# Performance work log

Hardware: AMD Instinct MI355X
Metric: run time of the kernel (lower is better)

## Reference

```python
import jax, jax.numpy as jnp
import numpy as np

H, C = 4, 32          # num_heads, hidden_channels
NEG_ATT = 0.2         # GAT attention leaky_relu slope (PyG default)
NEG_ACT = 0.01        # F.leaky_relu default slope applied after each conv


def gat_conv(x_src, x_dst, Wsrc, Wdst, a_src, a_dst, bias, src_idx, dst_idx, n_dst):
    """One bipartite GATConv (add_self_loops=False, concat=True)."""
    hs = (x_src @ Wsrc).reshape(-1, H, C)            # [Ns,H,C]
    hd = (x_dst @ Wdst).reshape(-1, H, C)            # [Nd,H,C]
    a_s = (hs * a_src).sum(-1)                       # [Ns,H]
    a_d = (hd * a_dst).sum(-1)                       # [Nd,H]
    e = jax.nn.leaky_relu(a_s[src_idx] + a_d[dst_idx], NEG_ATT)  # [E,H]
    m = jax.ops.segment_max(e, dst_idx, num_segments=n_dst)      # [Nd,H]
    ex = jnp.exp(e - m[dst_idx])
    denom = jax.ops.segment_sum(ex, dst_idx, num_segments=n_dst)
    alpha = ex / (denom[dst_idx] + 1e-16)            # edge softmax over dst
    msg = hs[src_idx] * alpha[:, :, None]            # [E,H,C]
    out = jax.ops.segment_sum(msg, dst_idx, num_segments=n_dst)  # [Nd,H,C]
    return out.reshape(n_dst, H * C) + bias


def setup_inputs() -> dict:
    key = jax.random.key(0)
    ks = jax.random.split(key, 40)
    it = iter(range(40))
    Nu, Nm, E, D, O = 100000, 20000, 500000, 64, 64
    HC = H * C

    def rn(shape, s=0.1):
        return jax.random.normal(ks[next(it)], shape, jnp.float32) * s

    def ri(n, hi):
        return jax.random.randint(ks[next(it)], (n,), 0, hi)

    return {
        "user_ids": jnp.arange(Nu), "movie_ids": jnp.arange(Nm),
        "um_src": ri(E, Nu), "um_dst": ri(E, Nm),
        "mu_src": ri(E, Nm), "mu_dst": ri(E, Nu),
        "user_emb": rn((Nu, D)), "movie_emb": rn((Nm, D)),
        "l1_um_Wsrc": rn((D, HC)), "l1_um_Wdst": rn((D, HC)),
        "l1_um_asrc": rn((H, C)), "l1_um_adst": rn((H, C)), "l1_um_b": rn((HC,)),
        "l1_mu_Wsrc": rn((D, HC)), "l1_mu_Wdst": rn((D, HC)),
        "l1_mu_asrc": rn((H, C)), "l1_mu_adst": rn((H, C)), "l1_mu_b": rn((HC,)),
        "l2_um_W": rn((HC, HC)), "l2_um_asrc": rn((H, C)), "l2_um_adst": rn((H, C)), "l2_um_b": rn((HC,)),
        "l2_mu_W": rn((HC, HC)), "l2_mu_asrc": rn((H, C)), "l2_mu_adst": rn((H, C)), "l2_mu_b": rn((HC,)),
        "Wo": rn((HC, O)), "bo": rn((O,)),
    }


def reference(user_ids, movie_ids, um_src, um_dst, mu_src, mu_dst,
              user_emb, movie_emb,
              l1_um_Wsrc, l1_um_Wdst, l1_um_asrc, l1_um_adst, l1_um_b,
              l1_mu_Wsrc, l1_mu_Wdst, l1_mu_asrc, l1_mu_adst, l1_mu_b,
              l2_um_W, l2_um_asrc, l2_um_adst, l2_um_b,
              l2_mu_W, l2_mu_asrc, l2_mu_adst, l2_mu_b,
              Wo, bo):
    xu = user_emb[user_ids]
    xm = movie_emb[movie_ids]
    Nu, Nm = xu.shape[0], xm.shape[0]
    # layer 1 (HeteroConv sum: each dst type receives exactly one edge type here)
    hm = gat_conv(xu, xm, l1_um_Wsrc, l1_um_Wdst, l1_um_asrc, l1_um_adst, l1_um_b, um_src, um_dst, Nm)
    hu = gat_conv(xm, xu, l1_mu_Wsrc, l1_mu_Wdst, l1_mu_asrc, l1_mu_adst, l1_mu_b, mu_src, mu_dst, Nu)
    xu = jax.nn.leaky_relu(hu, NEG_ACT)
    xm = jax.nn.leaky_relu(hm, NEG_ACT)
    # layer 2 (non-bipartite in_channels int => shared lin for src and dst)
    hm = gat_conv(xu, xm, l2_um_W, l2_um_W, l2_um_asrc, l2_um_adst, l2_um_b, um_src, um_dst, Nm)
    hu = gat_conv(xm, xu, l2_mu_W, l2_mu_W, l2_mu_asrc, l2_mu_adst, l2_mu_b, mu_src, mu_dst, Nu)
    xu = jax.nn.leaky_relu(hu, NEG_ACT)
    xm = jax.nn.leaky_relu(hm, NEG_ACT)
    out_user = xu @ Wo + bo
    out_movie = xm @ Wo + bo
    return out_user, out_movie, xu, xm
```

## Files before the change

kernel.cpp:

```cpp
#include <hip/hip_runtime.h>
#include <hip/hip_bf16.h>
#include <cstdint>


#define HC 128
#define HH 4
#define WPART 256
#define EPB 2048

typedef __attribute__((ext_vector_type(8))) short bf16x8;
typedef __attribute__((ext_vector_type(4))) float f32x4;

__device__ __forceinline__ short f2bf(float f) {
    return __builtin_bit_cast(short, __float2bfloat16(f));
}
__device__ __forceinline__ float bf2f(ushort u) {
    return __builtin_bit_cast(float, ((unsigned)u) << 16);
}

struct VT { const float* W[8]; const float* a[8]; float* v[8]; };
__global__ void make_v_all_k(VT t) {
    int gid = blockIdx.x * 256 + threadIdx.x;
    int task, base;
    if (gid < 1024) { task = gid >> 8; base = gid & 255; }
    else if (gid < 3072) { int g = gid - 1024; task = 4 + (g >> 9); base = g & 511; }
    else return;
    int k = base >> 2, h = base & 3;
    int coff = (task & 1) * 4;
    const float* wr = t.W[task] + (size_t)k * HC + h * 32;
    const float* ar = t.a[task] + h * 32;
    float s = 0.f;
    #pragma unroll
    for (int c = 0; c < 32; ++c) s = fmaf(wr[c], ar[c], s);
    t.v[task][k * 8 + coff + h] = s;
}

struct PT { const float* W[5]; const float* V[5]; ushort* Wb[5];
            int K[5]; int Nw[5]; int start[6]; };
__global__ void pack_all_k(PT t) {
    int gid = blockIdx.x * 256 + threadIdx.x;
    if (gid >= t.start[5]) return;
    int task = 0;
    while (gid >= t.start[task + 1]) ++task;
    int loc = gid - t.start[task];
    int K = t.K[task], Nw = t.Nw[task];
    int n = loc / K, k = loc % K;
    float v = 0.f;
    if (n < Nw) v = t.W[task][(size_t)k * Nw + n];
    else if (t.V[task] != nullptr && n < Nw + 8) v = t.V[task][k * 8 + (n - Nw)];
    t.Wb[task][loc] = (ushort)f2bf(v);
}

template <int NT, int MODE, bool ABF>
__global__ __launch_bounds__(256) void gemm_dual_k(
    const void* A0, const int* idx0, const ushort* Wb0, ushort* hsb0,
    ushort* atts0, float* attd0, float* C0, const float* bias0, int M0, int nb0,
    const void* A1, const int* idx1, const ushort* Wb1, ushort* hsb1,
    ushort* atts1, float* attd1, float* C1, const float* bias1, int M1,
    int K, int ldc) {
    const void* A; const int* aidx; const ushort* Wb; ushort* hsb;
    ushort* atts; float* attd; float* C; const float* bias; int M, bid;
    if ((int)blockIdx.x < nb0) {
        A = A0; aidx = idx0; Wb = Wb0; hsb = hsb0; atts = atts0; attd = attd0;
        C = C0; bias = bias0; M = M0; bid = blockIdx.x;
    } else {
        A = A1; aidx = idx1; Wb = Wb1; hsb = hsb1; atts = atts1; attd = attd1;
        C = C1; bias = bias1; M = M1; bid = blockIdx.x - nb0;
    }
    int lane = threadIdx.x & 63;
    int wave = threadIdx.x >> 6;
    int m_base = bid * 128 + wave * 32;
    int lm = lane & 15;
    int kg = lane >> 4;

    int r0 = m_base + lm, r1 = r0 + 16;
    int cr0 = r0 < M ? r0 : M - 1;
    int cr1 = r1 < M ? r1 : M - 1;
    int row0 = aidx ? aidx[cr0] : cr0;
    int row1 = aidx ? aidx[cr1] : cr1;
    const ushort* bp = Wb + (size_t)lm * K + kg * 8;

    f32x4 acc[2][NT] = {};
    for (int k0 = 0; k0 < K; k0 += 32) {
        bf16x8 a[2];
        if (ABF) {
            const ushort* a0p = (const ushort*)A + (size_t)row0 * K + kg * 8;
            const ushort* a1p = (const ushort*)A + (size_t)row1 * K + kg * 8;
            a[0] = *reinterpret_cast<const bf16x8*>(a0p + k0);
            a[1] = *reinterpret_cast<const bf16x8*>(a1p + k0);
        } else {
            const float* a0p = (const float*)A + (size_t)row0 * K + kg * 8;
            const float* a1p = (const float*)A + (size_t)row1 * K + kg * 8;
            float af[2][8];
            *reinterpret_cast<float4*>(&af[0][0]) = *reinterpret_cast<const float4*>(a0p + k0);
            *reinterpret_cast<float4*>(&af[0][4]) = *reinterpret_cast<const float4*>(a0p + k0 + 4);
            *reinterpret_cast<float4*>(&af[1][0]) = *reinterpret_cast<const float4*>(a1p + k0);
            *reinterpret_cast<float4*>(&af[1][4]) = *reinterpret_cast<const float4*>(a1p + k0 + 4);
            #pragma unroll
            for (int mi = 0; mi < 2; ++mi)
                #pragma unroll
                for (int j = 0; j < 8; ++j) a[mi][j] = f2bf(af[mi][j]);
        }
        #pragma unroll
        for (int nt = 0; nt < NT; ++nt) {
            bf16x8 b = *reinterpret_cast<const bf16x8*>(bp + (size_t)nt * 16 * K + k0);
            acc[0][nt] = __builtin_amdgcn_mfma_f32_16x16x32_bf16(a[0], b, acc[0][nt], 0, 0, 0);
            acc[1][nt] = __builtin_amdgcn_mfma_f32_16x16x32_bf16(a[1], b, acc[1][nt], 0, 0, 0);
        }
    }
    #pragma unroll
    for (int mi = 0; mi < 2; ++mi) {
        int rowb = m_base + mi * 16 + kg * 4;
        if (MODE == 0) {
            #pragma unroll
            for (int nt = 0; nt < NT - 1; ++nt) {
                int col = nt * 16 + lm;
                #pragma unroll
                for (int r = 0; r < 4; ++r) {
                    int row = rowb + r;
                    if (row < M) hsb[(size_t)row * HC + col] = (ushort)f2bf(acc[mi][nt][r]);
                }
            }
            #pragma unroll
            for (int r = 0; r < 4; ++r) {
                int row = rowb + r;
                if (row < M) {
                    float v = acc[mi][NT - 1][r];
                    if (lm < 4) atts[(size_t)row * 4 + lm] = (ushort)f2bf(v);
                    else if (lm < 8) attd[(size_t)row * 4 + (lm - 4)] = v;
                }
            }
        } else {
            #pragma unroll
            for (int nt = 0; nt < NT; ++nt) {
                int col = nt * 16 + lm;
                float bv = bias[col];
                #pragma unroll
                for (int r = 0; r < 4; ++r) {
                    int row = rowb + r;
                    if (row < M) C[(size_t)row * ldc + col] = acc[mi][nt][r] + bv;
                }
            }
        }
    }
}

__global__ __launch_bounds__(256) void part_count_k(
    const int* __restrict__ d0, int E0,
    const int* __restrict__ d1, int E1, int Nm,
    int* __restrict__ cntmat, int NB1) {
    __shared__ int lh[WPART];
    int t = threadIdx.x;
    lh[t] = 0;
    __syncthreads();
    int base = blockIdx.x * EPB + t;
    #pragma unroll
    for (int j = 0; j < EPB / 256; ++j) {
        int e = base + j * 256;
        int key = -1;
        if (e < E0) key = d0[e];
        else if (e - E0 < E1) key = Nm + d1[e - E0];
        if (key >= 0) atomicAdd(&lh[key >> 9], 1);
    }
    __syncthreads();
    cntmat[(size_t)t * NB1 + blockIdx.x] = lh[t];
}

__global__ __launch_bounds__(256) void part_scatter_k(
    const int* __restrict__ s0, const int* __restrict__ d0, int E0,
    const int* __restrict__ s1, const int* __restrict__ d1, int E1, int Nm,
    const int* __restrict__ scanned, int NB1, int2* __restrict__ buf) {
    __shared__ int lb[WPART];
    __shared__ int lc[WPART];
    int t = threadIdx.x;
    lb[t] = scanned[(size_t)t * NB1 + blockIdx.x];
    lc[t] = 0;
    __syncthreads();
    int base = blockIdx.x * EPB + t;
    #pragma unroll
    for (int j = 0; j < EPB / 256; ++j) {
        int e = base + j * 256;
        int key = -1, src = 0;
        if (e < E0) { key = d0[e]; src = s0[e]; }
        else if (e - E0 < E1) { key = Nm + d1[e - E0]; src = s1[e - E0]; }
        if (key >= 0) {
            int w = key >> 9;
            int r = atomicAdd(&lc[w], 1);
            buf[lb[w] + r] = make_int2(src, key);
        }
    }
}

__global__ __launch_bounds__(512) void csort_k(
    const int2* __restrict__ buf, const int* __restrict__ scanned, int NB1,
    int E, int NK, int* __restrict__ rs, int* __restrict__ csr) {
    __shared__ int c1[512];
    __shared__ int ls[512];
    int b = blockIdx.x;
    int t = threadIdx.x;
    int lo = scanned[(size_t)b * NB1];
    int hi = (b + 1 < WPART) ? scanned[(size_t)(b + 1) * NB1] : E;
    int keylo = b << 9;
    c1[t] = 0;
    __syncthreads();
    for (int i = lo + t; i < hi; i += 512)
        atomicAdd(&c1[buf[i].y - keylo], 1);
    __syncthreads();
    int v = c1[t];
    ls[t] = v;
    __syncthreads();
    for (int off = 1; off < 512; off <<= 1) {
        int x = (t >= off) ? ls[t - off] : 0;
        __syncthreads();
        ls[t] += x;
        __syncthreads();
    }
    ls[t] -= v;
    int gk = keylo + t;
    if (gk <= NK) rs[gk] = lo + ls[t];
    c1[t] = 0;
    __syncthreads();
    for (int i = lo + t; i < hi; i += 512) {
        int2 p = buf[i];
        int k = p.y - keylo;
        int r = atomicAdd(&c1[k], 1);
        csr[lo + ls[k] + r] = p.x;
    }
}

__global__ void scan_block_k(const int* __restrict__ deg, int n,
                             int* __restrict__ out, int* __restrict__ partial) {
    __shared__ int s[256];
    int i = blockIdx.x * 256 + threadIdx.x;
    int v = (i < n) ? deg[i] : 0;
    s[threadIdx.x] = v;
    __syncthreads();
    for (int off = 1; off < 256; off <<= 1) {
        int x = (threadIdx.x >= off) ? s[threadIdx.x - off] : 0;
        __syncthreads();
        s[threadIdx.x] += x;
        __syncthreads();
    }
    if (i < n) out[i] = s[threadIdx.x] - v;
    if (threadIdx.x == 255) partial[blockIdx.x] = s[255];
}

__global__ void scan_partial_k(int* __restrict__ partial, int nb) {
    __shared__ int s[512];
    int t = threadIdx.x;
    int v = (t < nb) ? partial[t] : 0;
    s[t] = v;
    __syncthreads();
    for (int off = 1; off < 512; off <<= 1) {
        int x = (t >= off) ? s[t - off] : 0;
        __syncthreads();
        s[t] += x;
        __syncthreads();
    }
    if (t < nb) partial[t] = s[t] - v;
}

__global__ void add_off_k(int* __restrict__ out, const int* __restrict__ partial, int n) {
    int i = blockIdx.x * 256 + threadIdx.x;
    if (i < n) out[i] += partial[blockIdx.x];
}

template <bool WF32, bool PROJ, bool GEMM2>
__global__ __launch_bounds__(256) void agg16_dual_k(
    const int* __restrict__ rs0, const int* __restrict__ csr0,
    const ushort* __restrict__ hsb0, const ushort* __restrict__ atts0,
    const float* __restrict__ attd0, const float* __restrict__ bias0,
    float* __restrict__ out0, int n0,
    const int* __restrict__ rs1, const int* __restrict__ csr1,
    const ushort* __restrict__ hsb1, const ushort* __restrict__ atts1,
    const float* __restrict__ attd1, const float* __restrict__ bias1,
    float* __restrict__ out1, int n1,
    const ushort* __restrict__ Wbo, const float* __restrict__ bo,
    float* __restrict__ pj0, float* __restrict__ pj1,
    const ushort* __restrict__ W2_0, ushort* __restrict__ hs2_0,
    ushort* __restrict__ atts2_0, float* __restrict__ attd2_0,
    const ushort* __restrict__ W2_1, ushort* __restrict__ hs2_1,
    ushort* __restrict__ atts2_1, float* __restrict__ attd2_1) {
    int blocksM = (n0 + 15) >> 4;
    bool ty1 = (int)blockIdx.x >= blocksM;
    int base = ty1 ? ((int)blockIdx.x - blocksM) * 16 : (int)blockIdx.x * 16;
    int gl = threadIdx.x >> 4;
    int c  = threadIdx.x & 15;
    int h  = c >> 2;
    const int* rs = ty1 ? rs1 : rs0;
    const int* csr = ty1 ? csr1 : csr0;
    const ushort* hsb = ty1 ? hsb1 : hsb0;
    const ushort* atts = ty1 ? atts1 : atts0;
    const float* attd = ty1 ? attd1 : attd0;
    const float* bias = ty1 ? bias1 : bias0;
    int n = ty1 ? n1 : n0;
    int node = base + gl;
    bool active = node < n;
    int nodeC = active ? node : 0;

    float ad = attd[nodeC * 4 + h];
    int s0 = 0, s1 = 0;
    if (active) { s0 = rs[nodeC]; s1 = rs[nodeC + 1]; }
    float acc[8] = {};
    float wsum = 0.f;
    int i = s0;
    for (; i + 4 <= s1; i += 4) {
        int sx[4];
        #pragma unroll
        for (int j = 0; j < 4; ++j) sx[j] = csr[i + j];
        bf16x8 hv[4]; float el[4];
        #pragma unroll
        for (int j = 0; j < 4; ++j) {
            hv[j] = *reinterpret_cast<const bf16x8*>(hsb + (size_t)sx[j] * HC + 8 * c);
            el[j] = bf2f(atts[(size_t)sx[j] * 4 + h]);
        }
        #pragma unroll
        for (int j = 0; j < 4; ++j) {
            float e = el[j] + ad;
            e = e > 0.f ? e : 0.2f * e;
            float w = __expf(e);
            wsum += w;
            #pragma unroll
            for (int k = 0; k < 8; ++k)
                acc[k] = fmaf(w, bf2f((ushort)hv[j][k]), acc[k]);
        }
    }
    for (; i < s1; ++i) {
        int src = csr[i];
        bf16x8 hv = *reinterpret_cast<const bf16x8*>(hsb + (size_t)src * HC + 8 * c);
        float e = bf2f(atts[(size_t)src * 4 + h]) + ad;
        e = e > 0.f ? e : 0.2f * e;
        float w = __expf(e);
        wsum += w;
        #pragma unroll
        for (int k = 0; k < 8; ++k)
            acc[k] = fmaf(w, bf2f((ushort)hv[k]), acc[k]);
    }
    float inv = 1.f / (wsum + 1e-16f);
    float v[8];
    #pragma unroll
    for (int k = 0; k < 8; ++k) {
        v[k] = fmaf(acc[k], inv, bias[8 * c + k]);
        v[k] = v[k] > 0.f ? v[k] : 0.01f * v[k];
    }
    if (WF32 && active) {
        float* out = ty1 ? out1 : out0;
        float4 o0 = make_float4(v[0], v[1], v[2], v[3]);
        float4 o1 = make_float4(v[4], v[5], v[6], v[7]);
        reinterpret_cast<float4*>(out + (size_t)node * HC + 8 * c)[0] = o0;
        reinterpret_cast<float4*>(out + (size_t)node * HC + 8 * c)[1] = o1;
    }
    if constexpr (PROJ || GEMM2) {
        __shared__ ushort As[16][136];
        bf16x8 u;
        #pragma unroll
        for (int k = 0; k < 8; ++k) u[k] = active ? f2bf(v[k]) : (short)0;
        *reinterpret_cast<bf16x8*>(&As[gl][8 * c]) = u;
        __syncthreads();
        int lane = threadIdx.x & 63;
        int wv = threadIdx.x >> 6;
        int lm = lane & 15;
        int kg = lane >> 4;
        if constexpr (PROJ) {
            int col = wv * 16 + lm;
            const ushort* bp = Wbo + (size_t)col * HC + kg * 8;
            f32x4 pacc = {};
            #pragma unroll
            for (int k0 = 0; k0 < HC; k0 += 32) {
                bf16x8 a = *reinterpret_cast<const bf16x8*>(&As[lm][k0 + kg * 8]);
                bf16x8 b = *reinterpret_cast<const bf16x8*>(bp + k0);
                pacc = __builtin_amdgcn_mfma_f32_16x16x32_bf16(a, b, pacc, 0, 0, 0);
            }
            float bv = bo[col];
            float* pj = ty1 ? pj1 : pj0;
            #pragma unroll
            for (int r = 0; r < 4; ++r) {
                int nd = base + kg * 4 + r;
                if (nd < n) pj[(size_t)nd * 64 + col] = pacc[r] + bv;
            }
        }
        if constexpr (GEMM2) {
            const ushort* W2 = ty1 ? W2_1 : W2_0;
            ushort* hs2 = ty1 ? hs2_1 : hs2_0;
            ushort* atts2 = ty1 ? atts2_1 : atts2_0;
            float* attd2 = ty1 ? attd2_1 : attd2_0;
            #pragma unroll
            for (int ti = 0; ti < 3; ++ti) {
                int t = wv + ti * 4;
                if (t > 8) break;
                int col = t * 16 + lm;
                const ushort* bp = W2 + (size_t)col * HC + kg * 8;
                f32x4 gacc = {};
                #pragma unroll
                for (int k0 = 0; k0 < HC; k0 += 32) {
                    bf16x8 a = *reinterpret_cast<const bf16x8*>(&As[lm][k0 + kg * 8]);
                    bf16x8 b = *reinterpret_cast<const bf16x8*>(bp + k0);
                    gacc = __builtin_amdgcn_mfma_f32_16x16x32_bf16(a, b, gacc, 0, 0, 0);
                }
                #pragma unroll
                for (int r = 0; r < 4; ++r) {
                    int nd = base + kg * 4 + r;
                    if (nd < n) {
                        if (t < 8) {
                            hs2[(size_t)nd * HC + col] = (ushort)f2bf(gacc[r]);
                        } else {
                            if (lm < 4) atts2[(size_t)nd * 4 + lm] = (ushort)f2bf(gacc[r]);
                            else if (lm < 8) attd2[(size_t)nd * 4 + (lm - 4)] = gacc[r];
                        }
                    }
                }
            }
        }
    }
}

extern "C" void kernel_launch(void* const* d_in, const int* in_sizes, int n_in,
                              void* d_out, int out_size, void* d_ws, size_t ws_size,
                              hipStream_t stream) {
    const int Nu = in_sizes[0];
    const int Nm = in_sizes[1];
    const int E1 = in_sizes[2];
    const int E2 = in_sizes[4];
    const int D  = in_sizes[6] / Nu;
    const int O  = in_sizes[27];
    const int E  = E1 + E2;
    const int NK = Nm + Nu;

    const int*   user_ids  = (const int*)d_in[0];
    const int*   movie_ids = (const int*)d_in[1];
    const int*   um_src    = (const int*)d_in[2];
    const int*   um_dst    = (const int*)d_in[3];
    const int*   mu_src    = (const int*)d_in[4];
    const int*   mu_dst    = (const int*)d_in[5];
    const float* user_emb  = (const float*)d_in[6];
    const float* movie_emb = (const float*)d_in[7];
    const float* l1_um_Wsrc = (const float*)d_in[8];
    const float* l1_um_Wdst = (const float*)d_in[9];
    const float* l1_um_asrc = (const float*)d_in[10];
    const float* l1_um_adst = (const float*)d_in[11];
    const float* l1_um_b    = (const float*)d_in[12];
    const float* l1_mu_Wsrc = (const float*)d_in[13];
    const float* l1_mu_Wdst = (const float*)d_in[14];
    const float* l1_mu_asrc = (const float*)d_in[15];
    const float* l1_mu_adst = (const float*)d_in[16];
    const float* l1_mu_b    = (const float*)d_in[17];
    const float* l2_um_W    = (const float*)d_in[18];
    const float* l2_um_asrc = (const float*)d_in[19];
    const float* l2_um_adst = (const float*)d_in[20];
    const float* l2_um_b    = (const float*)d_in[21];
    const float* l2_mu_W    = (const float*)d_in[22];
    const float* l2_mu_asrc = (const float*)d_in[23];
    const float* l2_mu_adst = (const float*)d_in[24];
    const float* l2_mu_b    = (const float*)d_in[25];
    const float* Wo         = (const float*)d_in[26];
    const float* bo         = (const float*)d_in[27];

    auto cdiv = [](int a, int b) { return (a + b - 1) / b; };
    const int NB1 = cdiv(E, EPB);
    const int CM  = WPART * NB1;

    char* p = (char*)d_ws;
    auto alloc = [&](size_t bytes) { void* r = p; p += (bytes + 255) & ~(size_t)255; return r; };
    ushort* hs_u  = (ushort*)alloc((size_t)Nu * HC * 2);
    ushort* hs_m  = (ushort*)alloc((size_t)Nm * HC * 2);
    ushort* hs_u2 = (ushort*)alloc((size_t)Nu * HC * 2);
    ushort* hs_m2 = (ushort*)alloc((size_t)Nm * HC * 2);
    ushort* atts_u  = (ushort*)alloc((size_t)Nu * 4 * 2);
    ushort* atts_m  = (ushort*)alloc((size_t)Nm * 4 * 2);
    ushort* atts_u2 = (ushort*)alloc((size_t)Nu * 4 * 2);
    ushort* atts_m2 = (ushort*)alloc((size_t)Nm * 4 * 2);
    float* attd_u  = (float*)alloc((size_t)Nu * 4 * 4);
    float* attd_m  = (float*)alloc((size_t)Nm * 4 * 4);
    float* attd_u2 = (float*)alloc((size_t)Nu * 4 * 4);
    float* attd_m2 = (float*)alloc((size_t)Nm * 4 * 4);
    float* V_u1  = (float*)alloc((size_t)HC * 8 * 4);
    float* V_m1  = (float*)alloc((size_t)HC * 8 * 4);
    float* V_u2  = (float*)alloc((size_t)HC * 8 * 4);
    float* V_m2  = (float*)alloc((size_t)HC * 8 * 4);
    ushort* Wb_u1 = (ushort*)alloc((size_t)144 * D * 2);
    ushort* Wb_m1 = (ushort*)alloc((size_t)144 * D * 2);
    ushort* Wb_u2 = (ushort*)alloc((size_t)144 * HC * 2);
    ushort* Wb_m2 = (ushort*)alloc((size_t)144 * HC * 2);
    ushort* Wb_o  = (ushort*)alloc((size_t)64 * HC * 2);
    int* rs      = (int*)alloc((size_t)(NK + 2) * 4);
    int* cntmat  = (int*)alloc((size_t)(CM + 256) * 4);
    int* scanned = (int*)alloc((size_t)(CM + 256) * 4);
    int2* buf    = (int2*)alloc((size_t)E * 8);
    int* csr     = (int*)alloc((size_t)E * 4);
    int* part    = (int*)alloc(1024 * 4);

    {
        VT vt;
        const float* Ws[8] = {l1_um_Wsrc, l1_mu_Wdst, l1_mu_Wsrc, l1_um_Wdst,
                              l2_um_W, l2_mu_W, l2_mu_W, l2_um_W};
        const float* as[8] = {l1_um_asrc, l1_mu_adst, l1_mu_asrc, l1_um_adst,
                              l2_um_asrc, l2_mu_adst, l2_mu_asrc, l2_um_adst};
        float* vs[8] = {V_u1, V_u1, V_m1, V_m1, V_u2, V_u2, V_m2, V_m2};
        for (int i = 0; i < 8; ++i) { vt.W[i] = Ws[i]; vt.a[i] = as[i]; vt.v[i] = vs[i]; }
        make_v_all_k<<<12, 256, 0, stream>>>(vt);

        PT pt;
        const float* pW[5] = {l1_um_Wsrc, l1_mu_Wsrc, l2_um_W, l2_mu_W, Wo};
        const float* pV[5] = {V_u1, V_m1, V_u2, V_m2, nullptr};
        ushort* pB[5] = {Wb_u1, Wb_m1, Wb_u2, Wb_m2, Wb_o};
        int pK[5] = {D, D, HC, HC, HC};
        int pN[5] = {HC, HC, HC, HC, 64};
        int cum = 0;
        for (int i = 0; i < 5; ++i) {
            pt.W[i] = pW[i]; pt.V[i] = pV[i]; pt.Wb[i] = pB[i];
            pt.K[i] = pK[i]; pt.Nw[i] = pN[i];
            pt.start[i] = cum;
            cum += (i < 4 ? 144 : 64) * pK[i];
        }
        pt.start[5] = cum;
        pack_all_k<<<cdiv(cum, 256), 256, 0, stream>>>(pt);
    }

    part_count_k<<<NB1, 256, 0, stream>>>(um_dst, E1, mu_dst, E2, Nm, cntmat, NB1);
    {
        int nb = cdiv(CM, 256);
        scan_block_k<<<nb, 256, 0, stream>>>(cntmat, CM, scanned, part);
        scan_partial_k<<<1, 512, 0, stream>>>(part, nb);
        add_off_k<<<nb, 256, 0, stream>>>(scanned, part, CM);
    }
    part_scatter_k<<<NB1, 256, 0, stream>>>(um_src, um_dst, E1, mu_src, mu_dst, E2,
                                            Nm, scanned, NB1, buf);
    csort_k<<<WPART, 512, 0, stream>>>(buf, scanned, NB1, E, NK, rs, csr);

    float* OU = (float*)d_out;
    float* OM = OU + (size_t)Nu * O;
    float* XU = OM + (size_t)Nm * O;
    float* XM = XU + (size_t)Nu * HC;

    int gbU = cdiv(Nu, 128), gbM = cdiv(Nm, 128);
    int aggBlocks = cdiv(Nm, 16) + cdiv(Nu, 16);

    gemm_dual_k<9, 0, false><<<gbU + gbM, 256, 0, stream>>>(
        user_emb, user_ids, Wb_u1, hs_u, atts_u, attd_u, nullptr, nullptr, Nu, gbU,
        movie_emb, movie_ids, Wb_m1, hs_m, atts_m, attd_m, nullptr, nullptr, Nm,
        D, 0);
    agg16_dual_k<false, false, true><<<aggBlocks, 256, 0, stream>>>(
        rs, csr, hs_u, atts_u, attd_m, l1_um_b, nullptr, Nm,
        rs + Nm, csr, hs_m, atts_m, attd_u, l1_mu_b, nullptr, Nu,
        nullptr, nullptr, nullptr, nullptr,
        Wb_m2, hs_m2, atts_m2, attd_m2,
        Wb_u2, hs_u2, atts_u2, attd_u2);

    agg16_dual_k<true, true, false><<<aggBlocks, 256, 0, stream>>>(
        rs, csr, hs_u2, atts_u2, attd_m2, l2_um_b, XM, Nm,
        rs + Nm, csr, hs_m2, atts_m2, attd_u2, l2_mu_b, XU, Nu,
        Wb_o, bo, OM, OU,
        nullptr, nullptr, nullptr, nullptr,
        nullptr, nullptr, nullptr, nullptr);
}
```

Before: 204.1 us.

## Process two destination nodes per 16-thread group in aggregation kernels

Each 16-lane group now aggregates two destination nodes at once, interleaving their gather loads so more independent memory requests are in flight. The block tile grows from 16 to 32 nodes, so the fused MFMA projection and layer-2 GEMM epilogue run two M-tiles per block and reuse each loaded weight fragment across both. The cost is higher register pressure from two accumulator sets and unequal degrees between the paired nodes causing divergent tail loops.

Result: slower. 208.9 us (+2.3%).

```diff
diff --git a/kernel.cpp b/kernel.cpp
--- a/kernel.cpp
+++ b/kernel.cpp
@@ -266,7 +266,7 @@
 }
 
 template <bool WF32, bool PROJ, bool GEMM2>
-__global__ __launch_bounds__(256) void agg16_dual_k(
+__global__ __launch_bounds__(256) void agg32_dual_k(
     const int* __restrict__ rs0, const int* __restrict__ csr0,
     const ushort* __restrict__ hsb0, const ushort* __restrict__ atts0,
     const float* __restrict__ attd0, const float* __restrict__ bias0,
@@ -281,9 +281,9 @@
     ushort* __restrict__ atts2_0, float* __restrict__ attd2_0,
     const ushort* __restrict__ W2_1, ushort* __restrict__ hs2_1,
     ushort* __restrict__ atts2_1, float* __restrict__ attd2_1) {
-    int blocksM = (n0 + 15) >> 4;
+    int blocksM = (n0 + 31) >> 5;
     bool ty1 = (int)blockIdx.x >= blocksM;
-    int base = ty1 ? ((int)blockIdx.x - blocksM) * 16 : (int)blockIdx.x * 16;
+    int base = ty1 ? ((int)blockIdx.x - blocksM) * 32 : (int)blockIdx.x * 32;
     int gl = threadIdx.x >> 4;
     int c  = threadIdx.x & 15;
     int h  = c >> 2;
@@ -294,20 +294,56 @@
     const float* attd = ty1 ? attd1 : attd0;
     const float* bias = ty1 ? bias1 : bias0;
     int n = ty1 ? n1 : n0;
-    int node = base + gl;
-    bool active = node < n;
-    int nodeC = active ? node : 0;
-
-    float ad = attd[nodeC * 4 + h];
-    int s0 = 0, s1 = 0;
-    if (active) { s0 = rs[nodeC]; s1 = rs[nodeC + 1]; }
-    float acc[8] = {};
-    float wsum = 0.f;
-    int i = s0;
-    for (; i + 4 <= s1; i += 4) {
+    int nA = base + 2 * gl, nB = nA + 1;
+    bool actA = nA < n, actB = nB < n;
+    int nAc = actA ? nA : 0, nBc = actB ? nB : 0;
+
+    float adA = attd[nAc * 4 + h];
+    float adB = attd[nBc * 4 + h];
+    int iA = 0, eA = 0, iB = 0, eB = 0;
+    if (actA) { iA = rs[nAc]; eA = rs[nAc + 1]; }
+    if (actB) { iB = rs[nBc]; eB = rs[nBc + 1]; }
+    float accA[8] = {}, accB[8] = {};
+    float wsA = 0.f, wsB = 0.f;
+
+    while (iA + 4 <= eA && iB + 4 <= eB) {
+        int sxA[4], sxB[4];
+        #pragma unroll
+        for (int j = 0; j < 4; ++j) { sxA[j] = csr[iA + j]; sxB[j] = csr[iB + j]; }
+        bf16x8 hvA[4], hvB[4]; float elA[4], elB[4];
+        #pragma unroll
+        for (int j = 0; j < 4; ++j) {
+            hvA[j] = *reinterpret_cast<const bf16x8*>(hsb + (size_t)sxA[j] * HC + 8 * c);
+            elA[j] = bf2f(atts[(size_t)sxA[j] * 4 + h]);
+            hvB[j] = *reinterpret_cast<const bf16x8*>(hsb + (size_t)sxB[j] * HC + 8 * c);
+            elB[j] = bf2f(atts[(size_t)sxB[j] * 4 + h]);
+        }
+        #pragma unroll
+        for (int j = 0; j < 4; ++j) {
+            float e = elA[j] + adA;
+            e = e > 0.f ? e : 0.2f * e;
+            float w = __expf(e);
+            wsA += w;
+            #pragma unroll
+            for (int k = 0; k < 8; ++k)
+                accA[k] = fmaf(w, bf2f((ushort)hvA[j][k]), accA[k]);
+        }
+        #pragma unroll
+        for (int j = 0; j < 4; ++j) {
+            float e = elB[j] + adB;
+            e = e > 0.f ? e : 0.2f * e;
+            float w = __expf(e);
+            wsB += w;
+            #pragma unroll
+            for (int k = 0; k < 8; ++k)
+                accB[k] = fmaf(w, bf2f((ushort)hvB[j][k]), accB[k]);
+        }
+        iA += 4; iB += 4;
+    }
+    for (; iA + 4 <= eA; iA += 4) {
         int sx[4];
         #pragma unroll
-        for (int j = 0; j < 4; ++j) sx[j] = csr[i + j];
+        for (int j = 0; j < 4; ++j) sx[j] = csr[iA + j];
         bf16x8 hv[4]; float el[4];
         #pragma unroll
         for (int j = 0; j < 4; ++j) {
@@ -316,46 +352,95 @@
         }
         #pragma unroll
         for (int j = 0; j < 4; ++j) {
-            float e = el[j] + ad;
+            float e = el[j] + adA;
             e = e > 0.f ? e : 0.2f * e;
             float w = __expf(e);
-            wsum += w;
+            wsA += w;
             #pragma unroll
             for (int k = 0; k < 8; ++k)
-                acc[k] = fmaf(w, bf2f((ushort)hv[j][k]), acc[k]);
-        }
-    }
-    for (; i < s1; ++i) {
-        int src = csr[i];
+                accA[k] = fmaf(w, bf2f((ushort)hv[j][k]), accA[k]);
+        }
+    }
+    for (; iB + 4 <= eB; iB += 4) {
+        int sx[4];
+        #pragma unroll
+        for (int j = 0; j < 4; ++j) sx[j] = csr[iB + j];
+        bf16x8 hv[4]; float el[4];
+        #pragma unroll
+        for (int j = 0; j < 4; ++j) {
+            hv[j] = *reinterpret_cast<const bf16x8*>(hsb + (size_t)sx[j] * HC + 8 * c);
+            el[j] = bf2f(atts[(size_t)sx[j] * 4 + h]);
+        }
+        #pragma unroll
+        for (int j = 0; j < 4; ++j) {
+            float e = el[j] + adB;
+            e = e > 0.f ? e : 0.2f * e;
+            float w = __expf(e);
+            wsB += w;
+            #pragma unroll
+            for (int k = 0; k < 8; ++k)
+                accB[k] = fmaf(w, bf2f((ushort)hv[j][k]), accB[k]);
+        }
+    }
+    for (; iA < eA; ++iA) {
+        int src = csr[iA];
         bf16x8 hv = *reinterpret_cast<const bf16x8*>(hsb + (size_t)src * HC + 8 * c);
-        float e = bf2f(atts[(size_t)src * 4 + h]) + ad;
+        float e = bf2f(atts[(size_t)src * 4 + h]) + adA;
         e = e > 0.f ? e : 0.2f * e;
         float w = __expf(e);
-        wsum += w;
+        wsA += w;
         #pragma unroll
         for (int k = 0; k < 8; ++k)
-            acc[k] = fmaf(w, bf2f((ushort)hv[k]), acc[k]);
-    }
-    float inv = 1.f / (wsum + 1e-16f);
-    float v[8];
+            accA[k] = fmaf(w, bf2f((ushort)hv[k]), accA[k]);
+    }
+    for (; iB < eB; ++iB) {
+        int src = csr[iB];
+        bf16x8 hv = *reinterpret_cast<const bf16x8*>(hsb + (size_t)src * HC + 8 * c);
+        float e = bf2f(atts[(size_t)src * 4 + h]) + adB;
+        e = e > 0.f ? e : 0.2f * e;
+        float w = __expf(e);
+        wsB += w;
+        #pragma unroll
+        for (int k = 0; k < 8; ++k)
+            accB[k] = fmaf(w, bf2f((ushort)hv[k]), accB[k]);
+    }
+
+    float invA = 1.f / (wsA + 1e-16f);
+    float invB = 1.f / (wsB + 1e-16f);
+    float vA[8], vB[8];
     #pragma unroll
     for (int k = 0; k < 8; ++k) {
-        v[k] = fmaf(acc[k], inv, bias[8 * c + k]);
-        v[k] = v[k] > 0.f ? v[k] : 0.01f * v[k];
-    }
-    if (WF32 && active) {
+        float bk = bias[8 * c + k];
+        vA[k] = fmaf(accA[k], invA, bk);
+        vA[k] = vA[k] > 0.f ? vA[k] : 0.01f * vA[k];
+        vB[k] = fmaf(accB[k], invB, bk);
+        vB[k] = vB[k] > 0.f ? vB[k] : 0.01f * vB[k];
+    }
+    if (WF32) {
         float* out = ty1 ? out1 : out0;
-        float4 o0 = make_float4(v[0], v[1], v[2], v[3]);
-        float4 o1 = make_float4(v[4], v[5], v[6], v[7]);
-        reinterpret_cast<float4*>(out + (size_t)node * HC + 8 * c)[0] = o0;
-        reinterpret_cast<float4*>(out + (size_t)node * HC + 8 * c)[1] = o1;
+        if (actA) {
+            reinterpret_cast<float4*>(out + (size_t)nA * HC + 8 * c)[0] =
+                make_float4(vA[0], vA[1], vA[2], vA[3]);
+            reinterpret_cast<float4*>(out + (size_t)nA * HC + 8 * c)[1] =
+                make_float4(vA[4], vA[5], vA[6], vA[7]);
+        }
+        if (actB) {
+            reinterpret_cast<float4*>(out + (size_t)nB * HC + 8 * c)[0] =
+                make_float4(vB[0], vB[1], vB[2], vB[3]);
+            reinterpret_cast<float4*>(out + (size_t)nB * HC + 8 * c)[1] =
+                make_float4(vB[4], vB[5], vB[6], vB[7]);
+        }
     }
     if constexpr (PROJ || GEMM2) {
-        __shared__ ushort As[16][136];
-        bf16x8 u;
-        #pragma unroll
-        for (int k = 0; k < 8; ++k) u[k] = active ? f2bf(v[k]) : (short)0;
-        *reinterpret_cast<bf16x8*>(&As[gl][8 * c]) = u;
+        __shared__ ushort As[32][136];
+        bf16x8 uA, uB;
+        #pragma unroll
+        for (int k = 0; k < 8; ++k) {
+            uA[k] = actA ? f2bf(vA[k]) : (short)0;
+            uB[k] = actB ? f2bf(vB[k]) : (short)0;
+        }
+        *reinterpret_cast<bf16x8*>(&As[2 * gl][8 * c]) = uA;
+        *reinterpret_cast<bf16x8*>(&As[2 * gl + 1][8 * c]) = uB;
         __syncthreads();
         int lane = threadIdx.x & 63;
         int wv = threadIdx.x >> 6;
@@ -364,19 +449,22 @@
         if constexpr (PROJ) {
             int col = wv * 16 + lm;
             const ushort* bp = Wbo + (size_t)col * HC + kg * 8;
-            f32x4 pacc = {};
-            #pragma unroll
-            for (int k0 = 0; k0 < HC; k0 += 32) {
-                bf16x8 a = *reinterpret_cast<const bf16x8*>(&As[lm][k0 + kg * 8]);
-                bf16x8 b = *reinterpret_cast<const bf16x8*>(bp + k0);
-                pacc = __builtin_amdgcn_mfma_f32_16x16x32_bf16(a, b, pacc, 0, 0, 0);
-            }
             float bv = bo[col];
             float* pj = ty1 ? pj1 : pj0;
             #pragma unroll
-            for (int r = 0; r < 4; ++r) {
-                int nd = base + kg * 4 + r;
-                if (nd < n) pj[(size_t)nd * 64 + col] = pacc[r] + bv;
+            for (int mi = 0; mi < 2; ++mi) {
+                f32x4 pacc = {};
+                #pragma unroll
+                for (int k0 = 0; k0 < HC; k0 += 32) {
+                    bf16x8 a = *reinterpret_cast<const bf16x8*>(&As[mi * 16 + lm][k0 + kg * 8]);
+                    bf16x8 b = *reinterpret_cast<const bf16x8*>(bp + k0);
+                    pacc = __builtin_amdgcn_mfma_f32_16x16x32_bf16(a, b, pacc, 0, 0, 0);
+                }
+                #pragma unroll
+                for (int r = 0; r < 4; ++r) {
+                    int nd = base + mi * 16 + kg * 4 + r;
+                    if (nd < n) pj[(size_t)nd * 64 + col] = pacc[r] + bv;
+                }
             }
         }
         if constexpr (GEMM2) {
@@ -390,22 +478,25 @@
                 if (t > 8) break;
                 int col = t * 16 + lm;
                 const ushort* bp = W2 + (size_t)col * HC + kg * 8;
-                f32x4 gacc = {};
                 #pragma unroll
-                for (int k0 = 0; k0 < HC; k0 += 32) {
-                    bf16x8 a = *reinterpret_cast<const bf16x8*>(&As[lm][k0 + kg * 8]);
-                    bf16x8 b = *reinterpret_cast<const bf16x8*>(bp + k0);
-                    gacc = __builtin_amdgcn_mfma_f32_16x16x32_bf16(a, b, gacc, 0, 0, 0);
-                }
-                #pragma unroll
-                for (int r = 0; r < 4; ++r) {
-                    int nd = base + kg * 4 + r;
-                    if (nd < n) {
-                        if (t < 8) {
-                            hs2[(size_t)nd * HC + col] = (ushort)f2bf(gacc[r]);
-                        } else {
-                            if (lm < 4) atts2[(size_t)nd * 4 + lm] = (ushort)f2bf(gacc[r]);
-                            else if (lm < 8) attd2[(size_t)nd * 4 + (lm - 4)] = gacc[r];
+                for (int mi = 0; mi < 2; ++mi) {
+                    f32x4 gacc = {};
+                    #pragma unroll
+                    for (int k0 = 0; k0 < HC; k0 += 32) {
+                        bf16x8 a = *reinterpret_cast<const bf16x8*>(&As[mi * 16 + lm][k0 + kg * 8]);
+                        bf16x8 b = *reinterpret_cast<const bf16x8*>(bp + k0);
+                        gacc = __builtin_amdgcn_mfma_f32_16x16x32_bf16(a, b, gacc, 0, 0, 0);
+                    }
+                    #pragma unroll
+                    for (int r = 0; r < 4; ++r) {
+                        int nd = base + mi * 16 + kg * 4 + r;
+                        if (nd < n) {
+                            if (t < 8) {
+                                hs2[(size_t)nd * HC + col] = (ushort)f2bf(gacc[r]);
+                            } else {
+                                if (lm < 4) atts2[(size_t)nd * 4 + lm] = (ushort)f2bf(gacc[r]);
+                                else if (lm < 8) attd2[(size_t)nd * 4 + (lm - 4)] = gacc[r];
+                            }
                         }
                     }
                 }
@@ -533,20 +624,20 @@
     float* XM = XU + (size_t)Nu * HC;
 
     int gbU = cdiv(Nu, 128), gbM = cdiv(Nm, 128);
-    int aggBlocks = cdiv(Nm, 16) + cdiv(Nu, 16);
+    int aggBlocks = cdiv(Nm, 32) + cdiv(Nu, 32);
 
     gemm_dual_k<9, 0, false><<<gbU + gbM, 256, 0, stream>>>(
         user_emb, user_ids, Wb_u1, hs_u, atts_u, attd_u, nullptr, nullptr, Nu, gbU,
         movie_emb, movie_ids, Wb_m1, hs_m, atts_m, attd_m, nullptr, nullptr, Nm,
         D, 0);
-    agg16_dual_k<false, false, true><<<aggBlocks, 256, 0, stream>>>(
+    agg32_dual_k<false, false, true><<<aggBlocks, 256, 0, stream>>>(
         rs, csr, hs_u, atts_u, attd_m, l1_um_b, nullptr, Nm,
         rs + Nm, csr, hs_m, atts_m, attd_u, l1_mu_b, nullptr, Nu,
         nullptr, nullptr, nullptr, nullptr,
         Wb_m2, hs_m2, atts_m2, attd_m2,
         Wb_u2, hs_u2, atts_u2, attd_u2);
 
-    agg16_dual_k<true, true, false><<<aggBlocks, 256, 0, stream>>>(
+    agg32_dual_k<true, true, false><<<aggBlocks, 256, 0, stream>>>(
         rs, csr, hs_u2, atts_u2, attd_m2, l2_um_b, XM, Nm,
         rs + Nm, csr, hs_m2, atts_m2, attd_u2, l2_mu_b, XU, Nu,
         Wb_o, bo, OM, OU,
```
